# Kernel optimization log

Measured on AMD Instinct MI355X. Metric: run time of the kernel, lower is better.

The kernel has to match this reference:

```python
import jax, jax.numpy as jnp
import numpy as np

B, H, S, D = 8, 8, 2048, 64
NEG = -1e9


def setup_inputs() -> dict:
    key = jax.random.key(0)
    k1, k2, k3, k4 = jax.random.split(key, 4)
    query = jax.random.normal(k1, (B, H, S, D), dtype=jnp.float32)
    kk = jax.random.normal(k2, (B, H, S, D), dtype=jnp.float32)
    value = jax.random.normal(k3, (B, H, S, D), dtype=jnp.float32)
    mask = jax.random.randint(k4, (B, S, S), 0, 2, dtype=jnp.int32)
    return {"query": query, "key": kk, "value": value, "mask": mask}


def reference(query, key, value, mask):
    dk = key.shape[-1]
    # scores: [B,H,S,S] = (q/sqrt(dk)) @ k^T
    scores = jnp.einsum('bhqd,bhkd->bhqk', query / np.sqrt(dk), key)
    # mask broadcast over heads: [B,1,S,S]
    scores = jnp.where(mask[:, None, :, :] == 0, NEG, scores)
    attn = jax.nn.softmax(scores.astype(jnp.float32), axis=-1).astype(query.dtype)
    # dropout is identity in eval/deterministic reference
    return jnp.einsum('bhqk,bhkd->bhqd', attn, value)
```

## Files before the change

kernel.cpp:

```cpp
#include <hip/hip_runtime.h>
#include <hip/hip_bf16.h>
#include <stdint.h>


#define B_ 8
#define H_ 8
#define S_ 2048
#define D_ 64
#define QT 128
#define KT 64
#define NT (S_ / KT)
#define TILE_E (KT * D_)
#define LOG2E 1.44269504088896340736f
#define QSCALE (0.125f * LOG2E)

typedef __bf16 bf16;
typedef bf16 bf16x8 __attribute__((ext_vector_type(8)));
typedef float f32x4 __attribute__((ext_vector_type(4)));
typedef unsigned short ushort8_t __attribute__((ext_vector_type(8)));
typedef unsigned long long u64;

#if __has_builtin(__builtin_amdgcn_exp2f)
#define EXP2(x) __builtin_amdgcn_exp2f(x)
#else
#define EXP2(x) exp2f(x)
#endif

static __device__ __forceinline__ unsigned short bfb(float f) {
    bf16 h = (bf16)f;
    return __builtin_bit_cast(unsigned short, h);
}
static __device__ __forceinline__ int phi_inv(int c) {
    return ((c >> 5) & 1) * 32 + ((c >> 2) & 1) * 16 + ((c >> 4) & 1) * 8 +
           ((c >> 3) & 1) * 4 + (c & 3);
}
static __device__ __forceinline__ void gload16(const unsigned short* g, unsigned short* l) {
    __builtin_amdgcn_global_load_lds(
        (const __attribute__((address_space(1))) unsigned int*)g,
        (__attribute__((address_space(3))) unsigned int*)l, 16, 0, 0);
}

#define KV_BLOCKS (B_ * H_ * NT)

__global__ __launch_bounds__(256) void prep_fused(
    const float* __restrict__ K, const float* __restrict__ V,
    unsigned short* __restrict__ Ko, unsigned short* __restrict__ Vo,
    const int* __restrict__ M, u64* __restrict__ W) {
    const int tid = threadIdx.x;
    if (blockIdx.x >= KV_BLOCKS) {
        const int ln = tid & 63;
        const int w0 = (blockIdx.x - KV_BLOCKS) * 32 + (tid >> 6) * 8;
#pragma unroll
        for (int j = 0; j < 8; ++j) {
            const int v = M[(long)(w0 + j) * 64 + ln];
            const u64 bal = __ballot(v != 0);
            if (ln == 0) W[w0 + j] = bal;
        }
        return;
    }
    if (Ko == nullptr) return;
    __shared__ float Vl[64][65];
    const int t = blockIdx.x & (NT - 1);
    const int bh = blockIdx.x >> 5;
    const float* Kg = K + ((long)bh * S_ + t * 64) * D_;
    const float* Vg = V + ((long)bh * S_ + t * 64) * D_;
    unsigned short* Kout = Ko + ((long)bh * S_ + t * 64) * D_;
    unsigned short* Vout = Vo + (long)bh * D_ * S_ + t * 64;
    {
        const int kv = tid >> 2, d0 = (tid & 3) * 16;
#pragma unroll
        for (int half = 0; half < 2; ++half) {
            const float4 f0 = *(const float4*)(Kg + kv * D_ + d0 + half * 8);
            const float4 f1 = *(const float4*)(Kg + kv * D_ + d0 + half * 8 + 4);
            ushort8_t u;
            u[0] = bfb(f0.x); u[1] = bfb(f0.y); u[2] = bfb(f0.z); u[3] = bfb(f0.w);
            u[4] = bfb(f1.x); u[5] = bfb(f1.y); u[6] = bfb(f1.z); u[7] = bfb(f1.w);
            *(ushort8_t*)(Kout + kv * D_ + d0 + half * 8) = u;
        }
    }
    {
#pragma unroll
        for (int i = 0; i < 4; ++i) {
            const int kv = i * 16 + (tid >> 4);
            const int d4 = (tid & 15) * 4;
            const float4 f = *(const float4*)(Vg + kv * D_ + d4);
            Vl[kv][d4 + 0] = f.x; Vl[kv][d4 + 1] = f.y;
            Vl[kv][d4 + 2] = f.z; Vl[kv][d4 + 3] = f.w;
        }
    }
    __syncthreads();
    {
#pragma unroll
        for (int j = 0; j < 4; ++j) {
            const int chunk = j * 256 + tid;
            const int d = chunk >> 4, q4 = chunk & 15;
            ushort4 w;
            w.x = bfb(Vl[phi_inv(q4 * 4 + 0)][d]);
            w.y = bfb(Vl[phi_inv(q4 * 4 + 1)][d]);
            w.z = bfb(Vl[phi_inv(q4 * 4 + 2)][d]);
            w.w = bfb(Vl[phi_inv(q4 * 4 + 3)][d]);
            *(ushort4*)(Vout + (long)d * S_ + q4 * 4) = w;
        }
    }
}

template <int MODE>
__global__ __launch_bounds__(512, 4) void attn_fwd(
    const float* __restrict__ Q, const float* __restrict__ K,
    const float* __restrict__ V, const int* __restrict__ M,
    const u64* __restrict__ W, const unsigned short* __restrict__ Kp,
    const unsigned short* __restrict__ Vp, float* __restrict__ O)
{
    __shared__ __attribute__((aligned(16))) unsigned short Ks3[4 * TILE_E];
    __shared__ __attribute__((aligned(16))) unsigned short Vt3[4 * TILE_E];

    const int tid = threadIdx.x;
    const int wv = tid >> 6, ln = tid & 63;
    const int col = ln & 15, grp = ln >> 4;

    int bid = blockIdx.x;
    bid = (bid & 7) * 128 + (bid >> 3);
    const int qt = bid & 15;
    const int h = (bid >> 4) & 7;
    const int b = bid >> 7;
    const int qw = qt * QT + wv * 16;

    const float* Qg = Q + ((long)((b * H_ + h) * S_) + qw + col) * D_;
    bf16x8 qf[2];
#pragma unroll
    for (int c = 0; c < 2; ++c) {
        const float4 a0 = *(const float4*)(Qg + c * 32 + grp * 8);
        const float4 a1 = *(const float4*)(Qg + c * 32 + grp * 8 + 4);
        qf[c][0] = (bf16)(a0.x * QSCALE); qf[c][1] = (bf16)(a0.y * QSCALE);
        qf[c][2] = (bf16)(a0.z * QSCALE); qf[c][3] = (bf16)(a0.w * QSCALE);
        qf[c][4] = (bf16)(a1.x * QSCALE); qf[c][5] = (bf16)(a1.y * QSCALE);
        qf[c][6] = (bf16)(a1.z * QSCALE); qf[c][7] = (bf16)(a1.w * QSCALE);
    }
    bf16x8 onesf;
#pragma unroll
    for (int j = 0; j < 8; ++j) onesf[j] = (bf16)1.0f;
    const f32x4 zq = (f32x4){0.f, 0.f, 0.f, 0.f};

    f32x4 oacc[4];
#pragma unroll
    for (int i = 0; i < 4; ++i) oacc[i] = zq;
    f32x4 accs = zq;

    const u64* Wg = (MODE >= 1) ? (W + ((long)b * S_ + qw + col) * (S_ / 64)) : nullptr;
    const int* Mg = (MODE == 0) ? (M + ((long)b * S_ + qw + col) * S_) : nullptr;
    const unsigned short* Kbh = Kp + (long)(b * H_ + h) * S_ * D_;
    const unsigned short* Vbh = Vp + (long)(b * H_ + h) * D_ * S_;
    const float* Kf = K + (long)(b * H_ + h) * S_ * D_;
    const float* Vf = V + (long)(b * H_ + h) * S_ * D_;

    const int rl = ln >> 3;
    const int c8 = (ln & 7) ^ rl;
    const int krow = wv * 8 + rl;

    float4 ka[2];
    float va[8];
    const int vd = ln, kg0 = wv;

    auto STAGE_ISSUE = [&](int kv0, int buf) {
        gload16(Kbh + (long)(kv0 + krow) * D_ + c8 * 8, Ks3 + buf * TILE_E + wv * 512);
        gload16(Vbh + (long)krow * S_ + kv0 + c8 * 8, Vt3 + buf * TILE_E + wv * 512);
    };
    auto LOADT = [&](int kv0) {
#pragma unroll
        for (int i = 0; i < 2; ++i) {
            const int idx4 = i * 512 + tid;
            const int row = idx4 >> 4, c4 = idx4 & 15;
            ka[i] = *(const float4*)(Kf + (long)(kv0 + row) * D_ + c4 * 4);
        }
#pragma unroll
        for (int i = 0; i < 2; ++i) {
            const int kg = kg0 + i * 8;
            const int kvn = phi_inv(kg * 4);
#pragma unroll
            for (int j = 0; j < 4; ++j)
                va[i * 4 + j] = Vf[(long)(kv0 + kvn + j) * D_ + vd];
        }
    };
    auto WRITET = [&](int buf) {
#pragma unroll
        for (int i = 0; i < 2; ++i) {
            const int idx4 = i * 512 + tid;
            const int row = idx4 >> 4, c4 = idx4 & 15;
            const int byte = (row * 128 + c4 * 8) ^ ((row & 7) << 4);
            ushort4 w;
            w.x = bfb(ka[i].x); w.y = bfb(ka[i].y);
            w.z = bfb(ka[i].z); w.w = bfb(ka[i].w);
            *(ushort4*)((char*)(Ks3 + buf * TILE_E) + byte) = w;
        }
#pragma unroll
        for (int i = 0; i < 2; ++i) {
            const int kg = kg0 + i * 8;
            const int byte = (vd * 128 + kg * 8) ^ ((vd & 7) << 4);
            ushort4 w;
            w.x = bfb(va[i * 4 + 0]); w.y = bfb(va[i * 4 + 1]);
            w.z = bfb(va[i * 4 + 2]); w.w = bfb(va[i * 4 + 3]);
            *(ushort4*)((char*)(Vt3 + buf * TILE_E) + byte) = w;
        }
    };

    auto STEP = [&](u64 mwfull, int t, const unsigned short* Kc, const unsigned short* Vc) {
        f32x4 sc[4];
        __builtin_amdgcn_s_setprio(1);
#pragma unroll
        for (int blk = 0; blk < 4; ++blk) {
            const int row = blk * 16 + col;
            const int byte0 = (row * 128 + grp * 16) ^ ((row & 7) << 4);
            const int byte1 = (row * 128 + 64 + grp * 16) ^ ((row & 7) << 4);
            const bf16x8 kf0 = *(const bf16x8*)((const char*)Kc + byte0);
            const bf16x8 kf1 = *(const bf16x8*)((const char*)Kc + byte1);
            sc[blk] = __builtin_amdgcn_mfma_f32_16x16x32_bf16(kf0, qf[0], zq, 0, 0, 0);
            sc[blk] = __builtin_amdgcn_mfma_f32_16x16x32_bf16(kf1, qf[1], sc[blk], 0, 0, 0);
        }
        __builtin_amdgcn_s_setprio(0);
        bf16x8 pf[2];
        if (MODE >= 1) {
            const u64 mws = mwfull >> (grp * 4);
            const unsigned mlo = (unsigned)mws, mhi = (unsigned)(mws >> 32);
#pragma unroll
            for (int c = 0; c < 2; ++c)
#pragma unroll
                for (int j = 0; j < 8; ++j) {
                    const int blk = 2 * c + (j >> 2), r = j & 3;
                    const unsigned w32 = (blk < 2) ? mlo : mhi;
                    const int bit = (blk & 1) * 16 + r;
                    const float s = ((w32 >> bit) & 1u) ? sc[blk][r] : -1e9f;
                    pf[c][j] = (bf16)EXP2(s);
                }
        } else {
#pragma unroll
            for (int c = 0; c < 2; ++c)
#pragma unroll
                for (int j = 0; j < 8; ++j) {
                    const int blk = 2 * c + (j >> 2), r = j & 3;
                    const int mv = Mg[t * KT + blk * 16 + grp * 4 + r];
                    const float s = mv ? sc[blk][r] : -1e9f;
                    pf[c][j] = (bf16)EXP2(s);
                }
        }
        __builtin_amdgcn_s_setprio(1);
        accs = __builtin_amdgcn_mfma_f32_16x16x32_bf16(pf[0], onesf, accs, 0, 0, 0);
        accs = __builtin_amdgcn_mfma_f32_16x16x32_bf16(pf[1], onesf, accs, 0, 0, 0);
#pragma unroll
        for (int c = 0; c < 2; ++c)
#pragma unroll
            for (int db = 0; db < 4; ++db) {
                const int vrow = db * 16 + col;
                const int byte = (vrow * 128 + c * 64 + grp * 16) ^ ((vrow & 7) << 4);
                const bf16x8 vf = *(const bf16x8*)((const char*)Vc + byte);
                oacc[db] = __builtin_amdgcn_mfma_f32_16x16x32_bf16(pf[c], vf, oacc[db], 0, 0, 0);
            }
        __builtin_amdgcn_s_setprio(0);
    };

#define WAIT2_BAR() do { asm volatile("s_waitcnt vmcnt(2)" ::: "memory"); \
    __builtin_amdgcn_s_barrier(); __builtin_amdgcn_sched_barrier(0); } while (0)
#define WAIT0_BAR() do { asm volatile("s_waitcnt vmcnt(0)" ::: "memory"); \
    __builtin_amdgcn_s_barrier(); __builtin_amdgcn_sched_barrier(0); } while (0)

    if (MODE == 2) {
        STAGE_ISSUE(0, 0);
        STAGE_ISSUE(KT, 1);
        WAIT2_BAR();
#pragma unroll 1
        for (int tt = 0; tt + 4 < NT; tt += 4) {
#pragma unroll
            for (int j = 0; j < 4; ++j) {
                const int t = tt + j;
                const u64 mw = Wg[t];
                STAGE_ISSUE((t + 2) * KT, (j + 2) & 3);
                STEP(mw, t, Ks3 + j * TILE_E, Vt3 + j * TILE_E);
                WAIT2_BAR();
            }
        }
        {
            const u64 mw0 = Wg[NT - 4];
            STAGE_ISSUE((NT - 2) * KT, (NT - 2) & 3);
            STEP(mw0, NT - 4, Ks3 + ((NT - 4) & 3) * TILE_E, Vt3 + ((NT - 4) & 3) * TILE_E);
            WAIT2_BAR();
            const u64 mw1 = Wg[NT - 3];
            STAGE_ISSUE((NT - 1) * KT, (NT - 1) & 3);
            STEP(mw1, NT - 3, Ks3 + ((NT - 3) & 3) * TILE_E, Vt3 + ((NT - 3) & 3) * TILE_E);
            WAIT2_BAR();
            const u64 mw2 = Wg[NT - 2];
            STEP(mw2, NT - 2, Ks3 + ((NT - 2) & 3) * TILE_E, Vt3 + ((NT - 2) & 3) * TILE_E);
            WAIT0_BAR();
            const u64 mw3 = Wg[NT - 1];
            STEP(mw3, NT - 1, Ks3 + ((NT - 1) & 3) * TILE_E, Vt3 + ((NT - 1) & 3) * TILE_E);
        }
    } else {
        LOADT(0);
        WRITET(0);
        __syncthreads();
#pragma unroll 1
        for (int t = 0; t < NT; t += 2) {
            if (t + 1 < NT) LOADT((t + 1) * KT);
            STEP(MODE >= 1 ? Wg[t] : 0ull, t, Ks3, Vt3);
            if (t + 1 < NT) WRITET(1);
            __syncthreads();
            if (t + 2 < NT) LOADT((t + 2) * KT);
            STEP(MODE >= 1 ? Wg[t + 1] : 0ull, t + 1, Ks3 + TILE_E, Vt3 + TILE_E);
            if (t + 2 < NT) WRITET(0);
            __syncthreads();
        }
    }

    float* Og = O + ((long)((b * H_ + h) * S_) + qw) * D_;
#pragma unroll
    for (int r = 0; r < 4; ++r) {
        const float inv = 1.0f / accs[r];
#pragma unroll
        for (int db = 0; db < 4; ++db)
            Og[(grp * 4 + r) * D_ + db * 16 + col] = oacc[db][r] * inv;
    }
#undef WAIT2_BAR
#undef WAIT0_BAR
}

extern "C" void kernel_launch(void* const* d_in, const int* in_sizes, int n_in,
                              void* d_out, int out_size, void* d_ws, size_t ws_size,
                              hipStream_t stream) {
    (void)in_sizes; (void)n_in; (void)out_size;
    const float* Q = (const float*)d_in[0];
    const float* K = (const float*)d_in[1];
    const float* V = (const float*)d_in[2];
    const int*   M = (const int*)d_in[3];
    float* O = (float*)d_out;

    const size_t szW = (size_t)B_ * S_ * (S_ / 64) * sizeof(u64);
    const size_t szK = (size_t)B_ * H_ * S_ * D_ * 2;
    const int grid = B_ * H_ * (S_ / QT);
    const int nmaskblk = (B_ * S_ * (S_ / 64)) / 32;

    if (ws_size >= szW + 2 * szK) {
        u64* W = (u64*)d_ws;
        unsigned short* Kp = (unsigned short*)((char*)d_ws + szW);
        unsigned short* Vp = (unsigned short*)((char*)d_ws + szW + szK);
        prep_fused<<<KV_BLOCKS + nmaskblk, 256, 0, stream>>>(K, V, Kp, Vp, M, W);
        attn_fwd<2><<<grid, 512, 0, stream>>>(Q, K, V, M, W, Kp, Vp, O);
    } else if (ws_size >= szW) {
        u64* W = (u64*)d_ws;
        prep_fused<<<KV_BLOCKS + nmaskblk, 256, 0, stream>>>(K, V, nullptr, nullptr, M, W);
        attn_fwd<1><<<grid, 512, 0, stream>>>(Q, K, V, M, W, nullptr, nullptr, O);
    } else {
        attn_fwd<0><<<grid, 512, 0, stream>>>(Q, K, V, M, nullptr, nullptr, nullptr, O);
    }
}
```

Before: 155.6 us.

## Software-pipeline QK of next tile with softmax-PV of current tile

The MODE 2 loop now splits each step into a QK^T stage and a softmax/PV stage. It computes the QK scores of tile t+1 while the exp and PV of tile t run, using ping-pong score registers and prefetching one tile further ahead (three in flight in a four-buffer ring). The mask is folded into the MFMA accumulator init as 0 or -1e9 additive bias, so no per-element select is needed after the matmul. This is meant to overlap MFMA latency with the exp work. It raises register pressure and lengthens the prologue and epilogue.

```diff
diff --git a/kernel.cpp b/kernel.cpp
--- a/kernel.cpp
+++ b/kernel.cpp
@@ -139,12 +139,11 @@
     bf16x8 onesf;
 #pragma unroll
     for (int j = 0; j < 8; ++j) onesf[j] = (bf16)1.0f;
-    const f32x4 zq = (f32x4){0.f, 0.f, 0.f, 0.f};
 
     f32x4 oacc[4];
 #pragma unroll
-    for (int i = 0; i < 4; ++i) oacc[i] = zq;
-    f32x4 accs = zq;
+    for (int i = 0; i < 4; ++i) oacc[i] = (f32x4){0.f, 0.f, 0.f, 0.f};
+    f32x4 accs = (f32x4){0.f, 0.f, 0.f, 0.f};
 
     const u64* Wg = (MODE >= 1) ? (W + ((long)b * S_ + qw + col) * (S_ / 64)) : nullptr;
     const int* Mg = (MODE == 0) ? (M + ((long)b * S_ + qw + col) * S_) : nullptr;
@@ -203,8 +202,18 @@
         }
     };
 
-    auto STEP = [&](u64 mwfull, int t, const unsigned short* Kc, const unsigned short* Vc) {
-        f32x4 sc[4];
+    auto QKB = [&](u64 mwfull, const unsigned short* Kc, f32x4* sc) {
+        const u64 mws = mwfull >> (grp * 4);
+        const unsigned mlo = (unsigned)mws, mhi = (unsigned)(mws >> 32);
+#pragma unroll
+        for (int blk = 0; blk < 4; ++blk) {
+            const unsigned w32 = (blk < 2) ? mlo : mhi;
+#pragma unroll
+            for (int r = 0; r < 4; ++r) {
+                const int bit = (blk & 1) * 16 + r;
+                sc[blk][r] = ((w32 >> bit) & 1u) ? 0.0f : -1e9f;
+            }
+        }
         __builtin_amdgcn_s_setprio(1);
 #pragma unroll
         for (int blk = 0; blk < 4; ++blk) {
@@ -213,35 +222,18 @@
             const int byte1 = (row * 128 + 64 + grp * 16) ^ ((row & 7) << 4);
             const bf16x8 kf0 = *(const bf16x8*)((const char*)Kc + byte0);
             const bf16x8 kf1 = *(const bf16x8*)((const char*)Kc + byte1);
-            sc[blk] = __builtin_amdgcn_mfma_f32_16x16x32_bf16(kf0, qf[0], zq, 0, 0, 0);
+            sc[blk] = __builtin_amdgcn_mfma_f32_16x16x32_bf16(kf0, qf[0], sc[blk], 0, 0, 0);
             sc[blk] = __builtin_amdgcn_mfma_f32_16x16x32_bf16(kf1, qf[1], sc[blk], 0, 0, 0);
         }
         __builtin_amdgcn_s_setprio(0);
+    };
+    auto SMPV = [&](f32x4* sc, const unsigned short* Vc) {
         bf16x8 pf[2];
-        if (MODE >= 1) {
-            const u64 mws = mwfull >> (grp * 4);
-            const unsigned mlo = (unsigned)mws, mhi = (unsigned)(mws >> 32);
-#pragma unroll
-            for (int c = 0; c < 2; ++c)
-#pragma unroll
-                for (int j = 0; j < 8; ++j) {
-                    const int blk = 2 * c + (j >> 2), r = j & 3;
-                    const unsigned w32 = (blk < 2) ? mlo : mhi;
-                    const int bit = (blk & 1) * 16 + r;
-                    const float s = ((w32 >> bit) & 1u) ? sc[blk][r] : -1e9f;
-                    pf[c][j] = (bf16)EXP2(s);
-                }
-        } else {
-#pragma unroll
-            for (int c = 0; c < 2; ++c)
-#pragma unroll
-                for (int j = 0; j < 8; ++j) {
-                    const int blk = 2 * c + (j >> 2), r = j & 3;
-                    const int mv = Mg[t * KT + blk * 16 + grp * 4 + r];
-                    const float s = mv ? sc[blk][r] : -1e9f;
-                    pf[c][j] = (bf16)EXP2(s);
-                }
-        }
+#pragma unroll
+        for (int c = 0; c < 2; ++c)
+#pragma unroll
+            for (int j = 0; j < 8; ++j)
+                pf[c][j] = (bf16)EXP2(sc[2 * c + (j >> 2)][j & 3]);
         __builtin_amdgcn_s_setprio(1);
         accs = __builtin_amdgcn_mfma_f32_16x16x32_bf16(pf[0], onesf, accs, 0, 0, 0);
         accs = __builtin_amdgcn_mfma_f32_16x16x32_bf16(pf[1], onesf, accs, 0, 0, 0);
@@ -263,47 +255,110 @@
     __builtin_amdgcn_s_barrier(); __builtin_amdgcn_sched_barrier(0); } while (0)
 
     if (MODE == 2) {
+        f32x4 scA[4], scB[4];
         STAGE_ISSUE(0, 0);
         STAGE_ISSUE(KT, 1);
         WAIT2_BAR();
+        {
+            const u64 mw0 = Wg[0];
+            QKB(mw0, Ks3, scA);
+            STAGE_ISSUE(2 * KT, 2);
+        }
+        WAIT2_BAR();
 #pragma unroll 1
-        for (int tt = 0; tt + 4 < NT; tt += 4) {
+        for (int tt = 0; tt < NT - 4; tt += 4) {
 #pragma unroll
             for (int j = 0; j < 4; ++j) {
                 const int t = tt + j;
-                const u64 mw = Wg[t];
-                STAGE_ISSUE((t + 2) * KT, (j + 2) & 3);
-                STEP(mw, t, Ks3 + j * TILE_E, Vt3 + j * TILE_E);
+                const u64 mwn = Wg[t + 1];
+                STAGE_ISSUE((t + 3) * KT, (j + 3) & 3);
+                if ((j & 1) == 0) {
+                    QKB(mwn, Ks3 + ((j + 1) & 3) * TILE_E, scB);
+                    SMPV(scA, Vt3 + j * TILE_E);
+                } else {
+                    QKB(mwn, Ks3 + ((j + 1) & 3) * TILE_E, scA);
+                    SMPV(scB, Vt3 + j * TILE_E);
+                }
                 WAIT2_BAR();
             }
         }
         {
-            const u64 mw0 = Wg[NT - 4];
-            STAGE_ISSUE((NT - 2) * KT, (NT - 2) & 3);
-            STEP(mw0, NT - 4, Ks3 + ((NT - 4) & 3) * TILE_E, Vt3 + ((NT - 4) & 3) * TILE_E);
+            const u64 mw29 = Wg[NT - 3];
+            STAGE_ISSUE((NT - 1) * KT, (NT - 1) & 3);
+            QKB(mw29, Ks3 + ((NT - 3) & 3) * TILE_E, scB);
+            SMPV(scA, Vt3 + ((NT - 4) & 3) * TILE_E);
             WAIT2_BAR();
-            const u64 mw1 = Wg[NT - 3];
-            STAGE_ISSUE((NT - 1) * KT, (NT - 1) & 3);
-            STEP(mw1, NT - 3, Ks3 + ((NT - 3) & 3) * TILE_E, Vt3 + ((NT - 3) & 3) * TILE_E);
-            WAIT2_BAR();
-            const u64 mw2 = Wg[NT - 2];
-            STEP(mw2, NT - 2, Ks3 + ((NT - 2) & 3) * TILE_E, Vt3 + ((NT - 2) & 3) * TILE_E);
+            const u64 mw30 = Wg[NT - 2];
+            QKB(mw30, Ks3 + ((NT - 2) & 3) * TILE_E, scA);
+            SMPV(scB, Vt3 + ((NT - 3) & 3) * TILE_E);
             WAIT0_BAR();
-            const u64 mw3 = Wg[NT - 1];
-            STEP(mw3, NT - 1, Ks3 + ((NT - 1) & 3) * TILE_E, Vt3 + ((NT - 1) & 3) * TILE_E);
+            const u64 mw31 = Wg[NT - 1];
+            QKB(mw31, Ks3 + ((NT - 1) & 3) * TILE_E, scB);
+            SMPV(scA, Vt3 + ((NT - 2) & 3) * TILE_E);
+            SMPV(scB, Vt3 + ((NT - 1) & 3) * TILE_E);
         }
     } else {
+        auto FSTEP = [&](u64 mwfull, int t, const unsigned short* Kc, const unsigned short* Vc) {
+            f32x4 sc[4];
+            const f32x4 zq = (f32x4){0.f, 0.f, 0.f, 0.f};
+#pragma unroll
+            for (int blk = 0; blk < 4; ++blk) {
+                const int row = blk * 16 + col;
+                const int byte0 = (row * 128 + grp * 16) ^ ((row & 7) << 4);
+                const int byte1 = (row * 128 + 64 + grp * 16) ^ ((row & 7) << 4);
+                const bf16x8 kf0 = *(const bf16x8*)((const char*)Kc + byte0);
+                const bf16x8 kf1 = *(const bf16x8*)((const char*)Kc + byte1);
+                sc[blk] = __builtin_amdgcn_mfma_f32_16x16x32_bf16(kf0, qf[0], zq, 0, 0, 0);
+                sc[blk] = __builtin_amdgcn_mfma_f32_16x16x32_bf16(kf1, qf[1], sc[blk], 0, 0, 0);
+            }
+            bf16x8 pf[2];
+            if (MODE >= 1) {
+                const u64 mws = mwfull >> (grp * 4);
+                const unsigned mlo = (unsigned)mws, mhi = (unsigned)(mws >> 32);
+#pragma unroll
+                for (int c = 0; c < 2; ++c)
+#pragma unroll
+                    for (int j = 0; j < 8; ++j) {
+                        const int blk = 2 * c + (j >> 2), r = j & 3;
+                        const unsigned w32 = (blk < 2) ? mlo : mhi;
+                        const int bit = (blk & 1) * 16 + r;
+                        const float s = ((w32 >> bit) & 1u) ? sc[blk][r] : -1e9f;
+                        pf[c][j] = (bf16)EXP2(s);
+                    }
+            } else {
+#pragma unroll
+                for (int c = 0; c < 2; ++c)
+#pragma unroll
+                    for (int j = 0; j < 8; ++j) {
+                        const int blk = 2 * c + (j >> 2), r = j & 3;
+                        const int mv = Mg[t * KT + blk * 16 + grp * 4 + r];
+                        const float s = mv ? sc[blk][r] : -1e9f;
+                        pf[c][j] = (bf16)EXP2(s);
+                    }
+            }
+            accs = __builtin_amdgcn_mfma_f32_16x16x32_bf16(pf[0], onesf, accs, 0, 0, 0);
+            accs = __builtin_amdgcn_mfma_f32_16x16x32_bf16(pf[1], onesf, accs, 0, 0, 0);
+#pragma unroll
+            for (int c = 0; c < 2; ++c)
+#pragma unroll
+                for (int db = 0; db < 4; ++db) {
+                    const int vrow = db * 16 + col;
+                    const int byte = (vrow * 128 + c * 64 + grp * 16) ^ ((vrow & 7) << 4);
+                    const bf16x8 vf = *(const bf16x8*)((const char*)Vc + byte);
+                    oacc[db] = __builtin_amdgcn_mfma_f32_16x16x32_bf16(pf[c], vf, oacc[db], 0, 0, 0);
+                }
+        };
         LOADT(0);
         WRITET(0);
         __syncthreads();
 #pragma unroll 1
         for (int t = 0; t < NT; t += 2) {
             if (t + 1 < NT) LOADT((t + 1) * KT);
-            STEP(MODE >= 1 ? Wg[t] : 0ull, t, Ks3, Vt3);
+            FSTEP(MODE >= 1 ? Wg[t] : 0ull, t, Ks3, Vt3);
             if (t + 1 < NT) WRITET(1);
             __syncthreads();
             if (t + 2 < NT) LOADT((t + 2) * KT);
-            STEP(MODE >= 1 ? Wg[t + 1] : 0ull, t + 1, Ks3 + TILE_E, Vt3 + TILE_E);
+            FSTEP(MODE >= 1 ? Wg[t + 1] : 0ull, t + 1, Ks3 + TILE_E, Vt3 + TILE_E);
             if (t + 2 < NT) WRITET(0);
             __syncthreads();
         }
```

After: 157.0 us. Within noise of the previous version (+0.9%).
